# Kernel optimization log

Measured on AMD Instinct MI355X. Metric: run time of the kernel, lower is better.

## Reference

```python
import jax, jax.numpy as jnp
import numpy as np

BN_EPS = 1e-5


def setup_inputs() -> dict:
    key = jax.random.key(0)
    ks = jax.random.split(key, 10)
    B, C, L = 16, 512, 1024
    scale = 1.0 / np.sqrt(C)
    inp = {
        "x": jax.random.normal(ks[0], (B, C, L), dtype=jnp.float32),
        "gamma": jnp.ones((C,), jnp.float32),
        "beta": jnp.zeros((C,), jnp.float32),
        "Wq": jax.random.normal(ks[1], (C, C), jnp.float32) * scale,
        "bq": jnp.zeros((C,), jnp.float32),
        "Wk": jax.random.normal(ks[2], (C, C), jnp.float32) * scale,
        "bk": jnp.zeros((C,), jnp.float32),
        "Wv": jax.random.normal(ks[3], (C, C), jnp.float32) * scale,
        "bv": jnp.zeros((C,), jnp.float32),
        "Wp": jax.random.normal(ks[4], (C, C), jnp.float32) * scale,
        "bp": jnp.zeros((C,), jnp.float32),
    }
    return inp


def _pointwise(W, b, h):
    # Conv1d with kernel_size=1 == per-position linear: [C_out,C_in] x [B,C_in,L]
    return jnp.einsum("oc,bcl->bol", W, h) + b[None, :, None]


def reference(x, gamma, beta, Wq, bq, Wk, bk, Wv, bv, Wp, bp):
    B, C, L = x.shape
    # BatchNorm1d (training-mode batch statistics over batch & length dims)
    mean = jnp.mean(x, axis=(0, 2), keepdims=True)
    var = jnp.var(x, axis=(0, 2), keepdims=True)
    hn = (x - mean) * jax.lax.rsqrt(var + BN_EPS)
    hn = hn * gamma[None, :, None] + beta[None, :, None]

    q = _pointwise(Wq, bq, hn)  # [B,C,L]
    k = _pointwise(Wk, bk, hn)
    v = _pointwise(Wv, bv, hn)

    # attn[b,i,j] = sum_c q[b,c,i] k[b,c,j] / sqrt(C); i=query pos, j=key pos
    attn = jnp.einsum("bci,bcj->bij", q, k) * (C ** -0.5)
    attn = jax.nn.softmax(attn, axis=-1)

    # out[b,c,i] = sum_j attn[b,i,j] v[b,c,j]
    h_ = jnp.einsum("bij,bcj->bci", attn, v)
    h_ = _pointwise(Wp, bp, h_)
    return x + h_
```

## Files before the change

kernel.cpp:

```cpp
#include <hip/hip_runtime.h>
#include <hip/hip_bf16.h>


#define BB 16
#define CC 512
#define LL 1024

typedef __bf16 bf16x8 __attribute__((ext_vector_type(8)));
typedef float  f32x4  __attribute__((ext_vector_type(4)));

__device__ inline unsigned short bf16_bits(float f) {
  __hip_bfloat16 h = __float2bfloat16(f);
  return __builtin_bit_cast(unsigned short, h);
}
__device__ inline float bits_lo(unsigned int u) {
  return __builtin_bit_cast(float, u << 16);
}
__device__ inline float bits_hi(unsigned int u) {
  return __builtin_bit_cast(float, u & 0xffff0000u);
}

__global__ __launch_bounds__(256) void bn_stats(
    const float* __restrict__ x, const float* __restrict__ gamma,
    const float* __restrict__ beta, float* __restrict__ scl,
    float* __restrict__ sft) {
  int c = blockIdx.x;
  int t = threadIdx.x;
  float s = 0.f, s2 = 0.f;
  for (int b = 0; b < BB; ++b) {
    float4 v = ((const float4*)(x + ((size_t)(b * CC + c)) * LL))[t];
    s  += v.x + v.y + v.z + v.w;
    s2 += v.x * v.x + v.y * v.y + v.z * v.z + v.w * v.w;
  }
  for (int m = 32; m; m >>= 1) { s += __shfl_xor(s, m, 64); s2 += __shfl_xor(s2, m, 64); }
  __shared__ float rs[4], rs2[4];
  int wave = t >> 6, lane = t & 63;
  if (lane == 0) { rs[wave] = s; rs2[wave] = s2; }
  __syncthreads();
  if (t == 0) {
    float S  = rs[0] + rs[1] + rs[2] + rs[3];
    float S2 = rs2[0] + rs2[1] + rs2[2] + rs2[3];
    float mean = S * (1.f / 16384.f);
    float var  = S2 * (1.f / 16384.f) - mean * mean;
    float sc = gamma[c] * rsqrtf(var + 1e-5f);
    scl[c] = sc;
    sft[c] = beta[c] - mean * sc;
  }
}

__global__ __launch_bounds__(256) void cast4(
    const float* __restrict__ Wq, const float* __restrict__ Wk,
    const float* __restrict__ Wv, const float* __restrict__ Wp,
    __hip_bfloat16* __restrict__ Wqkv, __hip_bfloat16* __restrict__ Wpb) {
  int m = blockIdx.y;
  const float* src = m == 0 ? Wq : m == 1 ? Wk : m == 2 ? Wv : Wp;
  __hip_bfloat16* dst = m < 3 ? Wqkv + (size_t)m * 262144 : Wpb;
  int i = blockIdx.x * 256 + threadIdx.x;
  float4 v = ((const float4*)src)[i];
  ushort4 o;
  o.x = bf16_bits(v.x); o.y = bf16_bits(v.y);
  o.z = bf16_bits(v.z); o.w = bf16_bits(v.w);
  ((ushort4*)dst)[i] = o;
}

__global__ __launch_bounds__(256) void norm_t(
    const float* __restrict__ x, const float* __restrict__ scl,
    const float* __restrict__ sft, __hip_bfloat16* __restrict__ hnT) {
  __shared__ float tile[32][33];
  int l0 = blockIdx.x * 32, c0 = blockIdx.y * 32, b = blockIdx.z;
  int t = threadIdx.x;
#pragma unroll
  for (int i = 0; i < 4; ++i) {
    int idx = t + i * 256;
    int cc = idx >> 5, ll = idx & 31;
    tile[cc][ll] = x[((size_t)(b * CC + c0 + cc)) * LL + l0 + ll];
  }
  __syncthreads();
#pragma unroll
  for (int i = 0; i < 2; ++i) {
    int idx = t + i * 256;
    int ll = idx >> 4, cc = (idx & 15) * 2;
    float v0 = tile[cc][ll] * scl[c0 + cc] + sft[c0 + cc];
    float v1 = tile[cc + 1][ll] * scl[c0 + cc + 1] + sft[c0 + cc + 1];
    ushort2 o; o.x = bf16_bits(v0); o.y = bf16_bits(v1);
    *(ushort2*)(hnT + ((size_t)(b * LL + l0 + ll)) * CC + c0 + cc) = o;
  }
}

__global__ __launch_bounds__(256) void softmax_bf16(__hip_bfloat16* __restrict__ S) {
  int wave = threadIdx.x >> 6, lane = threadIdx.x & 63;
  size_t row = (size_t)blockIdx.x * 4 + wave;
  uint4* p = (uint4*)(S + row * 1024);
  uint4 r0 = p[lane * 2], r1 = p[lane * 2 + 1];
  float f[16];
  unsigned int w[8] = {r0.x, r0.y, r0.z, r0.w, r1.x, r1.y, r1.z, r1.w};
#pragma unroll
  for (int i = 0; i < 8; ++i) { f[2 * i] = bits_lo(w[i]); f[2 * i + 1] = bits_hi(w[i]); }
  float mx = f[0];
#pragma unroll
  for (int i = 1; i < 16; ++i) mx = fmaxf(mx, f[i]);
  for (int m = 32; m; m >>= 1) mx = fmaxf(mx, __shfl_xor(mx, m, 64));
  float s = 0.f;
#pragma unroll
  for (int i = 0; i < 16; ++i) { f[i] = __expf(f[i] - mx); s += f[i]; }
  for (int m = 32; m; m >>= 1) s += __shfl_xor(s, m, 64);
  float inv = 1.f / s;
  unsigned int ow[8];
#pragma unroll
  for (int i = 0; i < 8; ++i) {
    unsigned int lo = bf16_bits(f[2 * i] * inv);
    unsigned int hi = bf16_bits(f[2 * i + 1] * inv);
    ow[i] = lo | (hi << 16);
  }
  uint4 o0 = {ow[0], ow[1], ow[2], ow[3]}, o1 = {ow[4], ow[5], ow[6], ow[7]};
  p[lane * 2] = o0; p[lane * 2 + 1] = o1;
}

__device__ __forceinline__ void gemm_core(
    const __hip_bfloat16* __restrict__ A, int lda,
    const __hip_bfloat16* __restrict__ B, int ldb, int K,
    __hip_bfloat16* sA, __hip_bfloat16* sB, f32x4 (&acc)[4][4]) {
  const int tid = threadIdx.x;
  const int wave = tid >> 6, lane = tid & 63;
  const int wm = (wave >> 1) * 64, wn = (wave & 1) * 64;
  const int row0 = tid >> 2;
  const int ke0 = (((tid & 3) ^ ((tid >> 3) & 3)) * 8);
  const int fr = lane & 15;
  const int q = lane >> 4;
  const int colA = ((q ^ ((fr >> 1) & 3)) * 8);
  for (int k0 = 0; k0 < K; k0 += 32) {
    __syncthreads();
#pragma unroll
    for (int it = 0; it < 2; ++it) {
      const __hip_bfloat16* ga = A + (size_t)(it * 64 + row0) * lda + (k0 + ke0);
      const __hip_bfloat16* gb = B + (size_t)(it * 64 + row0) * ldb + (k0 + ke0);
      __builtin_amdgcn_global_load_lds(
          (__attribute__((address_space(1))) void*)(void*)ga,
          (__attribute__((address_space(3))) void*)(sA + (it * 256 + wave * 64) * 8),
          16, 0, 0);
      __builtin_amdgcn_global_load_lds(
          (__attribute__((address_space(1))) void*)(void*)gb,
          (__attribute__((address_space(3))) void*)(sB + (it * 256 + wave * 64) * 8),
          16, 0, 0);
    }
    __syncthreads();
    bf16x8 af[4], bfr[4];
#pragma unroll
    for (int i = 0; i < 4; ++i) {
      af[i]  = *(const bf16x8*)(sA + (wm + i * 16 + fr) * 32 + colA);
      bfr[i] = *(const bf16x8*)(sB + (wn + i * 16 + fr) * 32 + colA);
    }
#pragma unroll
    for (int i = 0; i < 4; ++i)
#pragma unroll
      for (int j = 0; j < 4; ++j)
        acc[i][j] = __builtin_amdgcn_mfma_f32_16x16x32_bf16(af[i], bfr[j], acc[i][j], 0, 0, 0);
  }
}

__device__ __forceinline__ void gemm_core8p(
    const __hip_bfloat16* __restrict__ A, int lda,
    const __hip_bfloat16* __restrict__ B, int ldb, int K,
    __hip_bfloat16* sA, __hip_bfloat16* sB, f32x4 (&acc)[8][4]) {
  const int tid = threadIdx.x;
  const int wave = tid >> 6, lane = tid & 63;
  const int fr = lane & 15, q = lane >> 4;
  const int wm = (wave >> 2) * 128, wn = (wave & 3) * 64;
  const int srow = tid >> 3;
  const int sko = ((tid & 7) ^ (srow & 7)) * 8;
  const int NT = K >> 6;
  const int ck0 = (q ^ (fr & 7)) * 8;

#define STG_A(tt, u)                                                           \
  __builtin_amdgcn_global_load_lds(                                            \
      (__attribute__((address_space(1))) void*)(void*)(                        \
          A + (size_t)((u) * 64 + srow) * lda + (tt) * 64 + sko),              \
      (__attribute__((address_space(3))) void*)(                               \
          sA + ((tt) & 1) * 16384 + (u) * 4096 + wave * 512), 16, 0, 0)
#define STG_B(tt, u)                                                           \
  __builtin_amdgcn_global_load_lds(                                            \
      (__attribute__((address_space(1))) void*)(void*)(                        \
          B + (size_t)((u) * 64 + srow) * ldb + (tt) * 64 + sko),              \
      (__attribute__((address_space(3))) void*)(                               \
          sB + ((tt) & 1) * 16384 + (u) * 4096 + wave * 512), 16, 0, 0)

  STG_A(0, 0); STG_A(0, 1); STG_A(0, 2); STG_A(0, 3);
  STG_B(0, 0); STG_B(0, 1); STG_B(0, 2); STG_B(0, 3);
  STG_A(1, 0); STG_A(1, 1); STG_A(1, 2); STG_A(1, 3);
  STG_B(1, 0); STG_B(1, 1); STG_B(1, 2); STG_B(1, 3);

  for (int t = 0; t < NT; ++t) {
    const __hip_bfloat16* pA = sA + (t & 1) * 16384;
    const __hip_bfloat16* pB = sB + (t & 1) * 16384;
    const int rowA = wm + fr, rowB = wn + fr;
    const bool st = (t + 2) < NT;
    bf16x8 a03[4][2], a47[4][2], b01[2][2], b23[2][2];

    __builtin_amdgcn_sched_barrier(0);
    if (t == NT - 1) { asm volatile("s_waitcnt vmcnt(0)" ::: "memory"); }
    else             { asm volatile("s_waitcnt vmcnt(8)" ::: "memory"); }
    __builtin_amdgcn_s_barrier();
    __builtin_amdgcn_sched_barrier(0);

#pragma unroll
    for (int i = 0; i < 4; ++i) {
      a03[i][0] = *(const bf16x8*)(pA + (rowA + i * 16) * 64 + ck0);
      a03[i][1] = *(const bf16x8*)(pA + (rowA + i * 16) * 64 + (ck0 ^ 32));
    }
#pragma unroll
    for (int j = 0; j < 2; ++j) {
      b01[j][0] = *(const bf16x8*)(pB + (rowB + j * 16) * 64 + ck0);
      b01[j][1] = *(const bf16x8*)(pB + (rowB + j * 16) * 64 + (ck0 ^ 32));
    }
    __builtin_amdgcn_s_barrier();
    asm volatile("s_waitcnt lgkmcnt(0)" ::: "memory");
    __builtin_amdgcn_sched_barrier(0);
    __builtin_amdgcn_s_setprio(1);
#pragma unroll
    for (int i = 0; i < 4; ++i)
#pragma unroll
      for (int j = 0; j < 2; ++j) {
        acc[i][j] = __builtin_amdgcn_mfma_f32_16x16x32_bf16(a03[i][0], b01[j][0], acc[i][j], 0, 0, 0);
        acc[i][j] = __builtin_amdgcn_mfma_f32_16x16x32_bf16(a03[i][1], b01[j][1], acc[i][j], 0, 0, 0);
      }
    __builtin_amdgcn_s_setprio(0);
    __builtin_amdgcn_s_barrier();
    __builtin_amdgcn_sched_barrier(0);

#pragma unroll
    for (int j = 0; j < 2; ++j) {
      b23[j][0] = *(const bf16x8*)(pB + (rowB + 32 + j * 16) * 64 + ck0);
      b23[j][1] = *(const bf16x8*)(pB + (rowB + 32 + j * 16) * 64 + (ck0 ^ 32));
    }
    if (st) { STG_A(t + 2, 0); STG_A(t + 2, 2); }
    __builtin_amdgcn_s_barrier();
    asm volatile("s_waitcnt lgkmcnt(0)" ::: "memory");
    __builtin_amdgcn_sched_barrier(0);
    __builtin_amdgcn_s_setprio(1);
#pragma unroll
    for (int i = 0; i < 4; ++i)
#pragma unroll
      for (int j = 0; j < 2; ++j) {
        acc[i][2 + j] = __builtin_amdgcn_mfma_f32_16x16x32_bf16(a03[i][0], b23[j][0], acc[i][2 + j], 0, 0, 0);
        acc[i][2 + j] = __builtin_amdgcn_mfma_f32_16x16x32_bf16(a03[i][1], b23[j][1], acc[i][2 + j], 0, 0, 0);
      }
    __builtin_amdgcn_s_setprio(0);
    __builtin_amdgcn_s_barrier();
    __builtin_amdgcn_sched_barrier(0);

#pragma unroll
    for (int i = 0; i < 4; ++i) {
      a47[i][0] = *(const bf16x8*)(pA + (rowA + 64 + i * 16) * 64 + ck0);
      a47[i][1] = *(const bf16x8*)(pA + (rowA + 64 + i * 16) * 64 + (ck0 ^ 32));
    }
    if (st) { STG_B(t + 2, 0); STG_B(t + 2, 1); STG_B(t + 2, 2); }
    __builtin_amdgcn_s_barrier();
    asm volatile("s_waitcnt lgkmcnt(0)" ::: "memory");
    __builtin_amdgcn_sched_barrier(0);
    __builtin_amdgcn_s_setprio(1);
#pragma unroll
    for (int i = 0; i < 4; ++i)
#pragma unroll
      for (int j = 0; j < 2; ++j) {
        acc[4 + i][j] = __builtin_amdgcn_mfma_f32_16x16x32_bf16(a47[i][0], b01[j][0], acc[4 + i][j], 0, 0, 0);
        acc[4 + i][j] = __builtin_amdgcn_mfma_f32_16x16x32_bf16(a47[i][1], b01[j][1], acc[4 + i][j], 0, 0, 0);
      }
    __builtin_amdgcn_s_setprio(0);
    __builtin_amdgcn_s_barrier();
    __builtin_amdgcn_sched_barrier(0);

    if (st) { STG_B(t + 2, 3); STG_A(t + 2, 1); STG_A(t + 2, 3); }
    __builtin_amdgcn_s_barrier();
    __builtin_amdgcn_sched_barrier(0);
    __builtin_amdgcn_s_setprio(1);
#pragma unroll
    for (int i = 0; i < 4; ++i)
#pragma unroll
      for (int j = 0; j < 2; ++j) {
        acc[4 + i][2 + j] = __builtin_amdgcn_mfma_f32_16x16x32_bf16(a47[i][0], b23[j][0], acc[4 + i][2 + j], 0, 0, 0);
        acc[4 + i][2 + j] = __builtin_amdgcn_mfma_f32_16x16x32_bf16(a47[i][1], b23[j][1], acc[4 + i][2 + j], 0, 0, 0);
      }
    __builtin_amdgcn_s_setprio(0);
  }
#undef STG_A
#undef STG_B
}

__global__ __launch_bounds__(512, 2) void gemm_qkv256(
    const __hip_bfloat16* __restrict__ Wb, const __hip_bfloat16* __restrict__ hnT,
    __hip_bfloat16* __restrict__ qT, __hip_bfloat16* __restrict__ kT,
    __hip_bfloat16* __restrict__ vN,
    const float* __restrict__ bq, const float* __restrict__ bk,
    const float* __restrict__ bv) {
  __shared__ __align__(16) __hip_bfloat16 smem[4 * 16384];
  __hip_bfloat16* sA = smem;
  __hip_bfloat16* sB = smem + 32768;
  const int m0 = blockIdx.y * 256, n0 = blockIdx.x * 256;
  f32x4 acc[8][4] = {};
  gemm_core8p(Wb + (size_t)m0 * 512, 512, hnT + (size_t)n0 * 512, 512, 512,
              sA, sB, acc);
  const int tid = threadIdx.x;
  const int lane = tid & 63, wave = tid >> 6;
  const int wm = (wave >> 2) * 128, wn = (wave & 3) * 64;
  const int crow = (lane >> 4) * 4, ccol = lane & 15;
  const int id = m0 >> 9;
  const int mloc0 = (m0 & 511) + wm;
  const float* bias = id == 0 ? bq : id == 1 ? bk : bv;
  if (id < 2) {
    __hip_bfloat16* D = id == 0 ? qT : kT;
    const int mc0 = m0 & 511;
    __syncthreads();
#pragma unroll
    for (int h = 0; h < 2; ++h) {
      if ((wn >> 7) == h) {
        const int wnL = wn & 127;
#pragma unroll
        for (int i = 0; i < 8; ++i) {
          int mg = mloc0 + i * 16 + crow;
          int mr = wm + i * 16 + crow;
          float bv4[4];
#pragma unroll
          for (int r = 0; r < 4; ++r) bv4[r] = bias[mg + r];
#pragma unroll
          for (int j = 0; j < 4; ++j) {
            int colL = wnL + j * 16 + ccol;
            ushort4 o;
            o.x = bf16_bits(acc[i][j][0] + bv4[0]);
            o.y = bf16_bits(acc[i][j][1] + bv4[1]);
            o.z = bf16_bits(acc[i][j][2] + bv4[2]);
            o.w = bf16_bits(acc[i][j][3] + bv4[3]);
            *(ushort4*)(smem + colL * 264 + mr) = o;
          }
        }
      }
      __syncthreads();
#pragma unroll
      for (int rep = 0; rep < 8; ++rep) {
        int idx = rep * 512 + tid;
        int col = idx >> 5, c8 = idx & 31;
        bf16x8 v = *(const bf16x8*)(smem + col * 264 + c8 * 8);
        *(bf16x8*)(D + (size_t)(n0 + h * 128 + col) * 512 + mc0 + c8 * 8) = v;
      }
      __syncthreads();
    }
  } else {
#pragma unroll
    for (int i = 0; i < 8; ++i) {
      int mg = mloc0 + i * 16 + crow;
      float bv4[4];
#pragma unroll
      for (int r = 0; r < 4; ++r) bv4[r] = bias[mg + r];
#pragma unroll
      for (int j = 0; j < 4; ++j) {
        int ngf = n0 + wn + j * 16 + ccol;
        int b = ngf >> 10, l = ngf & 1023;
        __hip_bfloat16* D = vN + ((size_t)b * CC + mg) * LL + l;
#pragma unroll
        for (int r = 0; r < 4; ++r)
          D[(size_t)r * LL] = __float2bfloat16(acc[i][j][r] + bv4[r]);
      }
    }
  }
}

__global__ __launch_bounds__(512, 2) void gemm_s256(
    const __hip_bfloat16* __restrict__ qT, const __hip_bfloat16* __restrict__ kT,
    __hip_bfloat16* __restrict__ Sb) {
  __shared__ __align__(16) __hip_bfloat16 sA[2 * 16384];
  __shared__ __align__(16) __hip_bfloat16 sB[2 * 16384];
  const int bat = blockIdx.z;
  const int m0 = blockIdx.y * 256, n0 = blockIdx.x * 256;
  const size_t sLC = (size_t)LL * CC;
  f32x4 acc[8][4] = {};
  gemm_core8p(qT + (size_t)bat * sLC + (size_t)m0 * 512, 512,
              kT + (size_t)bat * sLC + (size_t)n0 * 512, 512, 512,
              sA, sB, acc);
  const int lane = threadIdx.x & 63, wave = threadIdx.x >> 6;
  const int wm = (wave >> 2) * 128, wn = (wave & 3) * 64;
  const int crow = (lane >> 4) * 4, ccol = lane & 15;
  __hip_bfloat16* D = Sb + (size_t)bat * LL * LL;
  const float scale = 0.04419417382415922f;
#pragma unroll
  for (int i = 0; i < 8; ++i) {
    int mg = m0 + wm + i * 16 + crow;
#pragma unroll
    for (int j = 0; j < 4; ++j) {
      int ng = n0 + wn + j * 16 + ccol;
#pragma unroll
      for (int r = 0; r < 4; ++r)
        D[(size_t)(mg + r) * LL + ng] = __float2bfloat16(acc[i][j][r] * scale);
    }
  }
}

template <int MODE, bool BIAS>
__global__ __launch_bounds__(256, 3) void gemm_tn(
    const __hip_bfloat16* __restrict__ A, int lda, size_t strideA,
    const __hip_bfloat16* __restrict__ B, int ldb, size_t strideB,
    void* __restrict__ Dp, int ldd, size_t strideD,
    const float* __restrict__ bias, float scale,
    const float* __restrict__ resid, size_t strideR, int K) {
  __shared__ __align__(16) __hip_bfloat16 sA[128 * 32];
  __shared__ __align__(16) __hip_bfloat16 sB[128 * 32];
  const int bat = blockIdx.z;
  const int m0 = blockIdx.y * 128, n0 = blockIdx.x * 128;
  f32x4 acc[4][4] = {};
  gemm_core(A + (size_t)bat * strideA + (size_t)m0 * lda, lda,
            B + (size_t)bat * strideB + (size_t)n0 * ldb, ldb, K, sA, sB, acc);
  const int lane = threadIdx.x & 63, wave = threadIdx.x >> 6;
  const int wm = (wave >> 1) * 64, wn = (wave & 1) * 64;
  const int crow = (lane >> 4) * 4, ccol = lane & 15;
  if constexpr (MODE == 0) {
    __hip_bfloat16* D = (__hip_bfloat16*)Dp + (size_t)bat * strideD;
#pragma unroll
    for (int i = 0; i < 4; ++i) {
      int mg = m0 + wm + i * 16 + crow;
      float bv4[4];
#pragma unroll
      for (int r = 0; r < 4; ++r) bv4[r] = BIAS ? bias[mg + r] : 0.f;
#pragma unroll
      for (int j = 0; j < 4; ++j) {
        int ng = n0 + wn + j * 16 + ccol;
#pragma unroll
        for (int r = 0; r < 4; ++r)
          D[(size_t)(mg + r) * ldd + ng] =
              __float2bfloat16(acc[i][j][r] * scale + bv4[r]);
      }
    }
  } else {
    float* D = (float*)Dp + (size_t)bat * strideD;
#pragma unroll
    for (int i = 0; i < 4; ++i) {
      int mg = m0 + wm + i * 16 + crow;
      float bv4[4];
#pragma unroll
      for (int r = 0; r < 4; ++r) bv4[r] = BIAS ? bias[mg + r] : 0.f;
#pragma unroll
      for (int j = 0; j < 4; ++j) {
        int ng = n0 + wn + j * 16 + ccol;
        const float* rsrc = resid + (size_t)bat * strideR + (size_t)mg * ldd + ng;
        float* dst = D + (size_t)mg * ldd + ng;
#pragma unroll
        for (int r = 0; r < 4; ++r)
          dst[(size_t)r * ldd] = acc[i][j][r] * scale + bv4[r] + rsrc[(size_t)r * ldd];
      }
    }
  }
}

extern "C" void kernel_launch(void* const* d_in, const int* in_sizes, int n_in,
                              void* d_out, int out_size, void* d_ws, size_t ws_size,
                              hipStream_t stream) {
  const float* x     = (const float*)d_in[0];
  const float* gamma = (const float*)d_in[1];
  const float* beta  = (const float*)d_in[2];
  const float* Wq    = (const float*)d_in[3];
  const float* bq    = (const float*)d_in[4];
  const float* Wk    = (const float*)d_in[5];
  const float* bk    = (const float*)d_in[6];
  const float* Wv    = (const float*)d_in[7];
  const float* bv    = (const float*)d_in[8];
  const float* Wp    = (const float*)d_in[9];
  const float* bp    = (const float*)d_in[10];
  float* out = (float*)d_out;

  char* ws = (char*)d_ws;
  float* scl = (float*)ws;
  float* sft = scl + 512;
  __hip_bfloat16* Wqkvb = (__hip_bfloat16*)(ws + 4096);
  __hip_bfloat16* Wpb = Wqkvb + 786432;
  __hip_bfloat16* hnT = Wpb + 262144;
  __hip_bfloat16* qT  = hnT + 8388608;
  __hip_bfloat16* kT  = qT + 8388608;
  __hip_bfloat16* vN  = kT + 8388608;
  __hip_bfloat16* Sb  = vN + 8388608;
  __hip_bfloat16* HT  = hnT;

  bn_stats<<<512, 256, 0, stream>>>(x, gamma, beta, scl, sft);
  cast4<<<dim3(256, 4), 256, 0, stream>>>(Wq, Wk, Wv, Wp, Wqkvb, Wpb);
  norm_t<<<dim3(32, 16, 16), 256, 0, stream>>>(x, scl, sft, hnT);

  const size_t sLC = (size_t)LL * CC;
  const size_t sCL = (size_t)CC * LL;
  const size_t sLLb = (size_t)LL * LL;

  gemm_qkv256<<<dim3(64, 6), 512, 0, stream>>>(Wqkvb, hnT, qT, kT, vN, bq, bk, bv);
  gemm_s256<<<dim3(4, 4, 16), 512, 0, stream>>>(qT, kT, Sb);
  softmax_bf16<<<4096, 256, 0, stream>>>(Sb);
  gemm_tn<0, false><<<dim3(4, 8, 16), 256, 0, stream>>>(
      Sb, 1024, sLLb, vN, 1024, sCL, HT, 512, sLC, nullptr, 1.f, nullptr, 0, 1024);
  gemm_tn<3, true><<<dim3(8, 4, 16), 256, 0, stream>>>(
      Wpb, 512, 0, HT, 512, sLC, out, 1024, sCL, bp, 1.f, x, sCL, 512);
}
```

Measured before the change: 235.4 us.

## Replace simple gemm_tn with double-buffered 256x128 pipelined core; flatten proj batch

```diff
diff --git a/kernel.cpp b/kernel.cpp
--- a/kernel.cpp
+++ b/kernel.cpp
@@ -116,48 +116,6 @@
   p[lane * 2] = o0; p[lane * 2 + 1] = o1;
 }
 
-__device__ __forceinline__ void gemm_core(
-    const __hip_bfloat16* __restrict__ A, int lda,
-    const __hip_bfloat16* __restrict__ B, int ldb, int K,
-    __hip_bfloat16* sA, __hip_bfloat16* sB, f32x4 (&acc)[4][4]) {
-  const int tid = threadIdx.x;
-  const int wave = tid >> 6, lane = tid & 63;
-  const int wm = (wave >> 1) * 64, wn = (wave & 1) * 64;
-  const int row0 = tid >> 2;
-  const int ke0 = (((tid & 3) ^ ((tid >> 3) & 3)) * 8);
-  const int fr = lane & 15;
-  const int q = lane >> 4;
-  const int colA = ((q ^ ((fr >> 1) & 3)) * 8);
-  for (int k0 = 0; k0 < K; k0 += 32) {
-    __syncthreads();
-#pragma unroll
-    for (int it = 0; it < 2; ++it) {
-      const __hip_bfloat16* ga = A + (size_t)(it * 64 + row0) * lda + (k0 + ke0);
-      const __hip_bfloat16* gb = B + (size_t)(it * 64 + row0) * ldb + (k0 + ke0);
-      __builtin_amdgcn_global_load_lds(
-          (__attribute__((address_space(1))) void*)(void*)ga,
-          (__attribute__((address_space(3))) void*)(sA + (it * 256 + wave * 64) * 8),
-          16, 0, 0);
-      __builtin_amdgcn_global_load_lds(
-          (__attribute__((address_space(1))) void*)(void*)gb,
-          (__attribute__((address_space(3))) void*)(sB + (it * 256 + wave * 64) * 8),
-          16, 0, 0);
-    }
-    __syncthreads();
-    bf16x8 af[4], bfr[4];
-#pragma unroll
-    for (int i = 0; i < 4; ++i) {
-      af[i]  = *(const bf16x8*)(sA + (wm + i * 16 + fr) * 32 + colA);
-      bfr[i] = *(const bf16x8*)(sB + (wn + i * 16 + fr) * 32 + colA);
-    }
-#pragma unroll
-    for (int i = 0; i < 4; ++i)
-#pragma unroll
-      for (int j = 0; j < 4; ++j)
-        acc[i][j] = __builtin_amdgcn_mfma_f32_16x16x32_bf16(af[i], bfr[j], acc[i][j], 0, 0, 0);
-  }
-}
-
 __device__ __forceinline__ void gemm_core8p(
     const __hip_bfloat16* __restrict__ A, int lda,
     const __hip_bfloat16* __restrict__ B, int ldb, int K,
@@ -281,6 +239,101 @@
         acc[4 + i][2 + j] = __builtin_amdgcn_mfma_f32_16x16x32_bf16(a47[i][1], b23[j][1], acc[4 + i][2 + j], 0, 0, 0);
       }
     __builtin_amdgcn_s_setprio(0);
+  }
+#undef STG_A
+#undef STG_B
+}
+
+__device__ __forceinline__ void gemm_core8p_n128(
+    const __hip_bfloat16* __restrict__ A, int lda,
+    const __hip_bfloat16* __restrict__ B, int ldb, int K,
+    __hip_bfloat16* sA, __hip_bfloat16* sB, f32x4 (&acc)[4][4]) {
+  const int tid = threadIdx.x;
+  const int wave = tid >> 6, lane = tid & 63;
+  const int fr = lane & 15, q = lane >> 4;
+  const int wm = (wave >> 1) * 64, wn = (wave & 1) * 64;
+  const int srow = tid >> 3;
+  const int sko = ((tid & 7) ^ (srow & 7)) * 8;
+  const int NT = K >> 6;
+  const int ck0 = (q ^ (fr & 7)) * 8;
+
+#define STG_A(tt, u)                                                           \
+  __builtin_amdgcn_global_load_lds(                                            \
+      (__attribute__((address_space(1))) void*)(void*)(                        \
+          A + (size_t)((u) * 64 + srow) * lda + (tt) * 64 + sko),              \
+      (__attribute__((address_space(3))) void*)(                               \
+          sA + ((tt) & 1) * 16384 + (u) * 4096 + wave * 512), 16, 0, 0)
+#define STG_B(tt, u)                                                           \
+  __builtin_amdgcn_global_load_lds(                                            \
+      (__attribute__((address_space(1))) void*)(void*)(                        \
+          B + (size_t)((u) * 64 + srow) * ldb + (tt) * 64 + sko),              \
+      (__attribute__((address_space(3))) void*)(                               \
+          sB + ((tt) & 1) * 8192 + (u) * 4096 + wave * 512), 16, 0, 0)
+
+  STG_A(0, 0); STG_A(0, 1); STG_A(0, 2); STG_A(0, 3); STG_B(0, 0); STG_B(0, 1);
+  STG_A(1, 0); STG_A(1, 1); STG_A(1, 2); STG_A(1, 3); STG_B(1, 0); STG_B(1, 1);
+
+  for (int t = 0; t < NT; ++t) {
+    const __hip_bfloat16* pA = sA + (t & 1) * 16384;
+    const __hip_bfloat16* pB = sB + (t & 1) * 8192;
+    const int rowA = wm + fr, rowB = wn + fr;
+    bf16x8 a01[2][2], a23[2][2], bfr[4][2];
+
+    __builtin_amdgcn_sched_barrier(0);
+    if (t == NT - 1) { asm volatile("s_waitcnt vmcnt(0)" ::: "memory"); }
+    else             { asm volatile("s_waitcnt vmcnt(6)" ::: "memory"); }
+    __builtin_amdgcn_s_barrier();
+    __builtin_amdgcn_sched_barrier(0);
+
+#pragma unroll
+    for (int i = 0; i < 2; ++i) {
+      a01[i][0] = *(const bf16x8*)(pA + (rowA + i * 16) * 64 + ck0);
+      a01[i][1] = *(const bf16x8*)(pA + (rowA + i * 16) * 64 + (ck0 ^ 32));
+    }
+#pragma unroll
+    for (int j = 0; j < 4; ++j) {
+      bfr[j][0] = *(const bf16x8*)(pB + (rowB + j * 16) * 64 + ck0);
+      bfr[j][1] = *(const bf16x8*)(pB + (rowB + j * 16) * 64 + (ck0 ^ 32));
+    }
+    __builtin_amdgcn_s_barrier();
+    asm volatile("s_waitcnt lgkmcnt(0)" ::: "memory");
+    __builtin_amdgcn_sched_barrier(0);
+    __builtin_amdgcn_s_setprio(1);
+#pragma unroll
+    for (int i = 0; i < 2; ++i)
+#pragma unroll
+      for (int j = 0; j < 4; ++j) {
+        acc[i][j] = __builtin_amdgcn_mfma_f32_16x16x32_bf16(a01[i][0], bfr[j][0], acc[i][j], 0, 0, 0);
+        acc[i][j] = __builtin_amdgcn_mfma_f32_16x16x32_bf16(a01[i][1], bfr[j][1], acc[i][j], 0, 0, 0);
+      }
+    __builtin_amdgcn_s_setprio(0);
+    __builtin_amdgcn_s_barrier();
+    __builtin_amdgcn_sched_barrier(0);
+
+#pragma unroll
+    for (int i = 0; i < 2; ++i) {
+      a23[i][0] = *(const bf16x8*)(pA + (rowA + 32 + i * 16) * 64 + ck0);
+      a23[i][1] = *(const bf16x8*)(pA + (rowA + 32 + i * 16) * 64 + (ck0 ^ 32));
+    }
+    __builtin_amdgcn_s_barrier();
+    asm volatile("s_waitcnt lgkmcnt(0)" ::: "memory");
+    __builtin_amdgcn_sched_barrier(0);
+    __builtin_amdgcn_s_setprio(1);
+#pragma unroll
+    for (int i = 0; i < 2; ++i)
+#pragma unroll
+      for (int j = 0; j < 4; ++j) {
+        acc[2 + i][j] = __builtin_amdgcn_mfma_f32_16x16x32_bf16(a23[i][0], bfr[j][0], acc[2 + i][j], 0, 0, 0);
+        acc[2 + i][j] = __builtin_amdgcn_mfma_f32_16x16x32_bf16(a23[i][1], bfr[j][1], acc[2 + i][j], 0, 0, 0);
+      }
+    __builtin_amdgcn_s_setprio(0);
+    __builtin_amdgcn_s_barrier();
+    __builtin_amdgcn_sched_barrier(0);
+
+    if ((t + 2) < NT) {
+      STG_A(t + 2, 0); STG_A(t + 2, 1); STG_A(t + 2, 2); STG_A(t + 2, 3);
+      STG_B(t + 2, 0); STG_B(t + 2, 1);
+    }
   }
 #undef STG_A
 #undef STG_B
@@ -394,19 +447,20 @@
 }
 
 template <int MODE, bool BIAS>
-__global__ __launch_bounds__(256, 3) void gemm_tn(
+__global__ __launch_bounds__(512, 2) void gemm_tn128(
     const __hip_bfloat16* __restrict__ A, int lda, size_t strideA,
     const __hip_bfloat16* __restrict__ B, int ldb, size_t strideB,
     void* __restrict__ Dp, int ldd, size_t strideD,
     const float* __restrict__ bias, float scale,
     const float* __restrict__ resid, size_t strideR, int K) {
-  __shared__ __align__(16) __hip_bfloat16 sA[128 * 32];
-  __shared__ __align__(16) __hip_bfloat16 sB[128 * 32];
+  __shared__ __align__(16) __hip_bfloat16 sA[2 * 16384];
+  __shared__ __align__(16) __hip_bfloat16 sB[2 * 8192];
   const int bat = blockIdx.z;
-  const int m0 = blockIdx.y * 128, n0 = blockIdx.x * 128;
+  const int m0 = blockIdx.y * 256, n0 = blockIdx.x * 128;
   f32x4 acc[4][4] = {};
-  gemm_core(A + (size_t)bat * strideA + (size_t)m0 * lda, lda,
-            B + (size_t)bat * strideB + (size_t)n0 * ldb, ldb, K, sA, sB, acc);
+  gemm_core8p_n128(A + (size_t)bat * strideA + (size_t)m0 * lda, lda,
+                   B + (size_t)bat * strideB + (size_t)n0 * ldb, ldb, K,
+                   sA, sB, acc);
   const int lane = threadIdx.x & 63, wave = threadIdx.x >> 6;
   const int wm = (wave >> 1) * 64, wn = (wave & 1) * 64;
   const int crow = (lane >> 4) * 4, ccol = lane & 15;
@@ -428,7 +482,7 @@
       }
     }
   } else {
-    float* D = (float*)Dp + (size_t)bat * strideD;
+    float* D = (float*)Dp;
 #pragma unroll
     for (int i = 0; i < 4; ++i) {
       int mg = m0 + wm + i * 16 + crow;
@@ -437,9 +491,10 @@
       for (int r = 0; r < 4; ++r) bv4[r] = BIAS ? bias[mg + r] : 0.f;
 #pragma unroll
       for (int j = 0; j < 4; ++j) {
-        int ng = n0 + wn + j * 16 + ccol;
-        const float* rsrc = resid + (size_t)bat * strideR + (size_t)mg * ldd + ng;
-        float* dst = D + (size_t)mg * ldd + ng;
+        int ngf = n0 + wn + j * 16 + ccol;
+        int b = ngf >> 10, l = ngf & 1023;
+        const float* rsrc = resid + (size_t)b * strideR + (size_t)mg * ldd + l;
+        float* dst = D + (size_t)b * strideD + (size_t)mg * ldd + l;
 #pragma unroll
         for (int r = 0; r < 4; ++r)
           dst[(size_t)r * ldd] = acc[i][j][r] * scale + bv4[r] + rsrc[(size_t)r * ldd];
@@ -487,8 +542,8 @@
   gemm_qkv256<<<dim3(64, 6), 512, 0, stream>>>(Wqkvb, hnT, qT, kT, vN, bq, bk, bv);
   gemm_s256<<<dim3(4, 4, 16), 512, 0, stream>>>(qT, kT, Sb);
   softmax_bf16<<<4096, 256, 0, stream>>>(Sb);
-  gemm_tn<0, false><<<dim3(4, 8, 16), 256, 0, stream>>>(
+  gemm_tn128<0, false><<<dim3(4, 4, 16), 512, 0, stream>>>(
       Sb, 1024, sLLb, vN, 1024, sCL, HT, 512, sLC, nullptr, 1.f, nullptr, 0, 1024);
-  gemm_tn<3, true><<<dim3(8, 4, 16), 256, 0, stream>>>(
-      Wpb, 512, 0, HT, 512, sLC, out, 1024, sCL, bp, 1.f, x, sCL, 512);
-}
+  gemm_tn128<3, true><<<dim3(128, 2, 1), 512, 0, stream>>>(
+      Wpb, 512, 0, HT, 512, 0, out, 1024, sCL, bp, 1.f, x, sCL, 512);
+}
```

After: 240.0 us. About the same (+1.9%).

## Fuse softmax exp into score GEMM and defer normalization to PV epilogue

Applied to the files above, without the earlier changes.

```diff
diff --git a/kernel.cpp b/kernel.cpp
--- a/kernel.cpp
+++ b/kernel.cpp
@@ -23,9 +23,11 @@
 __global__ __launch_bounds__(256) void bn_stats(
     const float* __restrict__ x, const float* __restrict__ gamma,
     const float* __restrict__ beta, float* __restrict__ scl,
-    float* __restrict__ sft) {
+    float* __restrict__ sft, float* __restrict__ rowsum) {
   int c = blockIdx.x;
   int t = threadIdx.x;
+  int g = c * 256 + t;
+  if (g < 16384) rowsum[g] = 0.f;
   float s = 0.f, s2 = 0.f;
   for (int b = 0; b < BB; ++b) {
     float4 v = ((const float4*)(x + ((size_t)(b * CC + c)) * LL))[t];
@@ -85,35 +87,6 @@
     ushort2 o; o.x = bf16_bits(v0); o.y = bf16_bits(v1);
     *(ushort2*)(hnT + ((size_t)(b * LL + l0 + ll)) * CC + c0 + cc) = o;
   }
-}
-
-__global__ __launch_bounds__(256) void softmax_bf16(__hip_bfloat16* __restrict__ S) {
-  int wave = threadIdx.x >> 6, lane = threadIdx.x & 63;
-  size_t row = (size_t)blockIdx.x * 4 + wave;
-  uint4* p = (uint4*)(S + row * 1024);
-  uint4 r0 = p[lane * 2], r1 = p[lane * 2 + 1];
-  float f[16];
-  unsigned int w[8] = {r0.x, r0.y, r0.z, r0.w, r1.x, r1.y, r1.z, r1.w};
-#pragma unroll
-  for (int i = 0; i < 8; ++i) { f[2 * i] = bits_lo(w[i]); f[2 * i + 1] = bits_hi(w[i]); }
-  float mx = f[0];
-#pragma unroll
-  for (int i = 1; i < 16; ++i) mx = fmaxf(mx, f[i]);
-  for (int m = 32; m; m >>= 1) mx = fmaxf(mx, __shfl_xor(mx, m, 64));
-  float s = 0.f;
-#pragma unroll
-  for (int i = 0; i < 16; ++i) { f[i] = __expf(f[i] - mx); s += f[i]; }
-  for (int m = 32; m; m >>= 1) s += __shfl_xor(s, m, 64);
-  float inv = 1.f / s;
-  unsigned int ow[8];
-#pragma unroll
-  for (int i = 0; i < 8; ++i) {
-    unsigned int lo = bf16_bits(f[2 * i] * inv);
-    unsigned int hi = bf16_bits(f[2 * i + 1] * inv);
-    ow[i] = lo | (hi << 16);
-  }
-  uint4 o0 = {ow[0], ow[1], ow[2], ow[3]}, o1 = {ow[4], ow[5], ow[6], ow[7]};
-  p[lane * 2] = o0; p[lane * 2 + 1] = o1;
 }
 
 __device__ __forceinline__ void gemm_core(
@@ -363,9 +336,9 @@
   }
 }
 
-__global__ __launch_bounds__(512, 2) void gemm_s256(
+__global__ __launch_bounds__(512, 2) void gemm_s256_exp(
     const __hip_bfloat16* __restrict__ qT, const __hip_bfloat16* __restrict__ kT,
-    __hip_bfloat16* __restrict__ Sb) {
+    __hip_bfloat16* __restrict__ Sb, float* __restrict__ rowsum) {
   __shared__ __align__(16) __hip_bfloat16 sA[2 * 16384];
   __shared__ __align__(16) __hip_bfloat16 sB[2 * 16384];
   const int bat = blockIdx.z;
@@ -379,16 +352,29 @@
   const int wm = (wave >> 2) * 128, wn = (wave & 3) * 64;
   const int crow = (lane >> 4) * 4, ccol = lane & 15;
   __hip_bfloat16* D = Sb + (size_t)bat * LL * LL;
+  float* rs = rowsum + (size_t)bat * LL;
   const float scale = 0.04419417382415922f;
 #pragma unroll
   for (int i = 0; i < 8; ++i) {
     int mg = m0 + wm + i * 16 + crow;
+    float sp[4] = {0.f, 0.f, 0.f, 0.f};
 #pragma unroll
     for (int j = 0; j < 4; ++j) {
       int ng = n0 + wn + j * 16 + ccol;
 #pragma unroll
-      for (int r = 0; r < 4; ++r)
-        D[(size_t)(mg + r) * LL + ng] = __float2bfloat16(acc[i][j][r] * scale);
+      for (int r = 0; r < 4; ++r) {
+        float e = __expf(acc[i][j][r] * scale);
+        sp[r] += e;
+        D[(size_t)(mg + r) * LL + ng] = __float2bfloat16(e);
+      }
+    }
+#pragma unroll
+    for (int r = 0; r < 4; ++r) {
+      for (int m = 8; m; m >>= 1) sp[r] += __shfl_xor(sp[r], m, 64);
+    }
+    if (ccol == 0) {
+#pragma unroll
+      for (int r = 0; r < 4; ++r) atomicAdd(&rs[mg + r], sp[r]);
     }
   }
 }
@@ -399,7 +385,8 @@
     const __hip_bfloat16* __restrict__ B, int ldb, size_t strideB,
     void* __restrict__ Dp, int ldd, size_t strideD,
     const float* __restrict__ bias, float scale,
-    const float* __restrict__ resid, size_t strideR, int K) {
+    const float* __restrict__ resid, size_t strideR,
+    const float* __restrict__ rowdiv, int K) {
   __shared__ __align__(16) __hip_bfloat16 sA[128 * 32];
   __shared__ __align__(16) __hip_bfloat16 sB[128 * 32];
   const int bat = blockIdx.z;
@@ -425,6 +412,24 @@
         for (int r = 0; r < 4; ++r)
           D[(size_t)(mg + r) * ldd + ng] =
               __float2bfloat16(acc[i][j][r] * scale + bv4[r]);
+      }
+    }
+  } else if constexpr (MODE == 1) {
+    __hip_bfloat16* D = (__hip_bfloat16*)Dp + (size_t)bat * strideD;
+    const float* rsb = rowdiv + (size_t)bat * LL;
+#pragma unroll
+    for (int i = 0; i < 4; ++i) {
+      int mg = m0 + wm + i * 16 + crow;
+      float rinv[4];
+#pragma unroll
+      for (int r = 0; r < 4; ++r) rinv[r] = 1.f / rsb[mg + r];
+#pragma unroll
+      for (int j = 0; j < 4; ++j) {
+        int ng = n0 + wn + j * 16 + ccol;
+#pragma unroll
+        for (int r = 0; r < 4; ++r)
+          D[(size_t)(mg + r) * ldd + ng] =
+              __float2bfloat16(acc[i][j][r] * rinv[r]);
       }
     }
   } else {
@@ -474,9 +479,10 @@
   __hip_bfloat16* kT  = qT + 8388608;
   __hip_bfloat16* vN  = kT + 8388608;
   __hip_bfloat16* Sb  = vN + 8388608;
+  float* rowsum = (float*)(Sb + 16777216);
   __hip_bfloat16* HT  = hnT;
 
-  bn_stats<<<512, 256, 0, stream>>>(x, gamma, beta, scl, sft);
+  bn_stats<<<512, 256, 0, stream>>>(x, gamma, beta, scl, sft, rowsum);
   cast4<<<dim3(256, 4), 256, 0, stream>>>(Wq, Wk, Wv, Wp, Wqkvb, Wpb);
   norm_t<<<dim3(32, 16, 16), 256, 0, stream>>>(x, scl, sft, hnT);
 
@@ -485,10 +491,10 @@
   const size_t sLLb = (size_t)LL * LL;
 
   gemm_qkv256<<<dim3(64, 6), 512, 0, stream>>>(Wqkvb, hnT, qT, kT, vN, bq, bk, bv);
-  gemm_s256<<<dim3(4, 4, 16), 512, 0, stream>>>(qT, kT, Sb);
-  softmax_bf16<<<4096, 256, 0, stream>>>(Sb);
-  gemm_tn<0, false><<<dim3(4, 8, 16), 256, 0, stream>>>(
-      Sb, 1024, sLLb, vN, 1024, sCL, HT, 512, sLC, nullptr, 1.f, nullptr, 0, 1024);
+  gemm_s256_exp<<<dim3(4, 4, 16), 512, 0, stream>>>(qT, kT, Sb, rowsum);
+  gemm_tn<1, false><<<dim3(4, 8, 16), 256, 0, stream>>>(
+      Sb, 1024, sLLb, vN, 1024, sCL, HT, 512, sLC, nullptr, 1.f, nullptr, 0,
+      rowsum, 1024);
   gemm_tn<3, true><<<dim3(8, 4, 16), 256, 0, stream>>>(
-      Wpb, 512, 0, HT, 512, sLC, out, 1024, sCL, bp, 1.f, x, sCL, 512);
-}
+      Wpb, 512, 0, HT, 512, sLC, out, 1024, sCL, bp, 1.f, x, sCL, nullptr, 512);
+}
```

After: 226.7 us. -3.7%, faster.
